# Kernel optimization log

Measured on AMD Instinct MI355X. Metric: run time of the kernel, lower is better.

Reference implementation:

```python
import jax, jax.numpy as jnp
import numpy as np

B = 256          # games in flight
BS = 19          # board side
N2 = BS * BS     # 361 points
M = N2 * 10      # history_factor = 10 -> max moves = 3610


def setup_inputs() -> dict:
    key = jax.random.key(0)
    k = jax.random.split(key, 8)
    legal_mask = jax.random.bernoulli(k[0], 0.5, (B, BS, BS))
    # captures are sparse: few stones captured per candidate move
    capture_stone_mask = jax.random.bernoulli(k[1], 0.02, (B, N2, N2))
    current_player = jax.random.randint(k[2], (B,), 0, 2, dtype=jnp.int32)
    zpos = jax.random.randint(k[3], (N2, 3), 0, 2**31 - 1, dtype=jnp.int32)
    current_hash = jax.random.randint(k[4], (B,), 0, 2**31 - 1, dtype=jnp.int32)
    hash_history = jax.random.randint(k[5], (B, M), 0, 2**31 - 1, dtype=jnp.int32)
    move_count = jax.random.randint(k[6], (B,), 0, M, dtype=jnp.int32)
    logits = jax.random.normal(k[7], (B, BS, BS), dtype=jnp.float32)
    return dict(legal_mask=legal_mask, capture_stone_mask=capture_stone_mask,
                current_player=current_player, zpos=zpos,
                current_hash=current_hash, hash_history=hash_history,
                move_count=move_count, logits=logits)


def _super_ko_filter(legal_mask, capture_stone_mask, current_player, zpos,
                     current_hash, hash_history, move_count):
    Bb, H, W = legal_mask.shape
    n2 = H * W
    legal_flat = legal_mask.reshape(Bb, n2)                      # (B, N2)
    player = current_player.astype(jnp.int32)                    # (B,)
    zposT = zpos.T                                               # (3, N2)

    # 1) delta for placing the stone: empty-key XOR player-key
    place_old = zposT[0][None, :]                                # (1, N2)
    place_new = zposT[player + 1]                                # (B, N2) gather per-batch
    place_delta = jnp.bitwise_xor(place_old, place_new)          # (B, N2)

    # 2) delta for removing a captured opponent stone at each point
    z_opp = zposT[2 - player]                                    # opp+1 = 2-player, (B, N2)
    D = jnp.bitwise_xor(z_opp, zposT[0][None, :])                # (B, N2)

    # per candidate move, XOR the deltas of all stones it would capture
    sel = jnp.where(capture_stone_mask, D[:, None, :], jnp.int32(0))  # (B, N2, N2)
    cap_delta = jax.lax.reduce(sel, jnp.int32(0), jax.lax.bitwise_xor, (2,))  # (B, N2)

    # 3) post-move hash per candidate
    new_hash = current_hash[:, None] ^ place_delta ^ cap_delta   # (B, N2)

    # 4) reject if post-move hash appears in the (valid prefix of) history
    hist_mask = jnp.arange(hash_history.shape[1])[None, :] < move_count[:, None]  # (B, M)
    eq = (new_hash[:, :, None] == hash_history[:, None, :]) & hist_mask[:, None, :]
    is_repeat = jnp.any(eq, axis=2) & legal_flat                 # (B, N2)

    return legal_mask & ~is_repeat.reshape(Bb, H, W)


def reference(legal_mask, capture_stone_mask, current_player, zpos,
              current_hash, hash_history, move_count, logits):
    final_mask = _super_ko_filter(legal_mask, capture_stone_mask, current_player,
                                  zpos, current_hash, hash_history, move_count)
    # downstream use of the filtered mask: mask policy logits
    return jnp.where(final_mask, logits, jnp.float32(-1e9))
```

## Files before the change

kernel.cpp:

```cpp
#include <hip/hip_runtime.h>
#include <stdint.h>


#define GO_B   256
#define GO_N2  361
#define GO_M   3610
#define TBL    1024
#define BTHR   512

__global__ __launch_bounds__(256)
void scan_kernel(const int* __restrict__ cap,
                 const int* __restrict__ player,
                 const int* __restrict__ zpos,
                 uint32_t*  __restrict__ capx_out)
{
    const int b    = blockIdx.x >> 2;
    const int g    = blockIdx.x & 3;
    const int wid  = g * 4 + (threadIdx.x >> 6);
    const int lane = threadIdx.x & 63;
    const int p    = player[b];

    uint32_t D[6];
    #pragma unroll
    for (int s = 0; s < 6; ++s) {
        int j = lane + 64 * s;
        D[s] = (j < GO_N2)
             ? ((uint32_t)zpos[j * 3 + 0] ^ (uint32_t)zpos[j * 3 + 2 - p])
             : 0u;
    }

    const int* __restrict__ base_b = cap + (size_t)b * GO_N2 * GO_N2;

    for (int i = wid; i < GO_N2; i += 32) {
        const int  iB   = i + 16;
        const bool hasB = (iB < GO_N2);
        const int* __restrict__ rowA = base_b + (size_t)i  * GO_N2;
        const int* __restrict__ rowB = base_b + (size_t)iB * GO_N2;

        uint32_t a0, a1, a2, a3, a4, a5;
        uint32_t b0, b1, b2, b3, b4, b5;
        a0 = (uint32_t)rowA[lane];
        a1 = (uint32_t)rowA[lane + 64];
        a2 = (uint32_t)rowA[lane + 128];
        a3 = (uint32_t)rowA[lane + 192];
        a4 = (uint32_t)rowA[lane + 256];
        a5 = (lane + 320 < GO_N2) ? (uint32_t)rowA[lane + 320] : 0u;
        b0 = hasB ? (uint32_t)rowB[lane]       : 0u;
        b1 = hasB ? (uint32_t)rowB[lane + 64]  : 0u;
        b2 = hasB ? (uint32_t)rowB[lane + 128] : 0u;
        b3 = hasB ? (uint32_t)rowB[lane + 192] : 0u;
        b4 = hasB ? (uint32_t)rowB[lane + 256] : 0u;
        b5 = (hasB && lane + 320 < GO_N2) ? (uint32_t)rowB[lane + 320] : 0u;

        uint32_t accA = (a0 ? D[0] : 0u) ^ (a1 ? D[1] : 0u) ^ (a2 ? D[2] : 0u)
                      ^ (a3 ? D[3] : 0u) ^ (a4 ? D[4] : 0u) ^ (a5 ? D[5] : 0u);
        uint32_t accB = (b0 ? D[0] : 0u) ^ (b1 ? D[1] : 0u) ^ (b2 ? D[2] : 0u)
                      ^ (b3 ? D[3] : 0u) ^ (b4 ? D[4] : 0u) ^ (b5 ? D[5] : 0u);

        #pragma unroll
        for (int off = 32; off >= 1; off >>= 1) {
            accA ^= __shfl_xor(accA, off, 64);
            accB ^= __shfl_xor(accB, off, 64);
        }
        if (lane == 0) {
            capx_out[(size_t)b * GO_N2 + i] = accA;
            if (hasB) capx_out[(size_t)b * GO_N2 + iB] = accB;
        }
    }
}

__global__ __launch_bounds__(BTHR)
void finalize_kernel(const int*      __restrict__ legal,
                     const int*      __restrict__ player,
                     const int*      __restrict__ zpos,
                     const int*      __restrict__ chash,
                     const int*      __restrict__ hist,
                     const int*      __restrict__ mcount,
                     const float*    __restrict__ logits,
                     const uint32_t* __restrict__ capx,
                     float*          __restrict__ out)
{
    __shared__ uint32_t thash[TBL];
    __shared__ int      tidx[TBL];
    __shared__ uint8_t  rep[GO_N2];
    __shared__ uint8_t  leg[GO_N2];

    const int b   = blockIdx.x;
    const int tid = threadIdx.x;
    const int p   = player[b];
    const uint32_t ch = (uint32_t)chash[b];

    for (int s = tid; s < TBL; s += BTHR) tidx[s] = -1;
    for (int i = tid; i < GO_N2; i += BTHR) {
        rep[i] = 0u;
        leg[i] = legal[(size_t)b * GO_N2 + i] != 0;
    }
    __syncthreads();

    for (int i = tid; i < GO_N2; i += BTHR) {
        uint32_t z0 = (uint32_t)zpos[i * 3 + 0];
        uint32_t zp = (uint32_t)zpos[i * 3 + 1 + p];
        uint32_t nh = ch ^ (z0 ^ zp) ^ capx[(size_t)b * GO_N2 + i];
        if (leg[i]) {
            uint32_t s = nh & (TBL - 1);
            while (true) {
                int prev = atomicCAS(&tidx[s], -1, i);
                if (prev == -1) { thash[s] = nh; break; }
                s = (s + 1) & (TBL - 1);
            }
        }
    }
    __syncthreads();

    const int mc = mcount[b];
    for (int m = tid; m < mc; m += BTHR) {
        uint32_t h = (uint32_t)hist[(size_t)b * GO_M + m];
        uint32_t s = h & (TBL - 1);
        while (tidx[s] != -1) {
            if (thash[s] == h) rep[tidx[s]] = 1u;
            s = (s + 1) & (TBL - 1);
        }
    }
    __syncthreads();

    for (int i = tid; i < GO_N2; i += BTHR) {
        bool keep = leg[i] && !rep[i];
        out[(size_t)b * GO_N2 + i] =
            keep ? logits[(size_t)b * GO_N2 + i] : -1.0e9f;
    }
}

extern "C" void kernel_launch(void* const* d_in, const int* in_sizes, int n_in,
                              void* d_out, int out_size, void* d_ws, size_t ws_size,
                              hipStream_t stream) {
    const int*   legal  = (const int*)d_in[0];
    const int*   cap    = (const int*)d_in[1];
    const int*   player = (const int*)d_in[2];
    const int*   zpos   = (const int*)d_in[3];
    const int*   chash  = (const int*)d_in[4];
    const int*   hist   = (const int*)d_in[5];
    const int*   mcount = (const int*)d_in[6];
    const float* logits = (const float*)d_in[7];
    float*       outp   = (float*)d_out;
    uint32_t*    capx   = (uint32_t*)d_ws;

    scan_kernel<<<GO_B * 4, 256, 0, stream>>>(cap, player, zpos, capx);
    finalize_kernel<<<GO_B, BTHR, 0, stream>>>(legal, player, zpos, chash,
                                               hist, mcount, logits, capx, outp);
}
```

Before: 237.9 us.

## Stage capture-mask rows through LDS tiles with contiguous loads in scan kernel

```diff
diff --git a/kernel.cpp b/kernel.cpp
--- a/kernel.cpp
+++ b/kernel.cpp
@@ -2,70 +2,80 @@
 #include <stdint.h>
 
 
-#define GO_B   256
-#define GO_N2  361
-#define GO_M   3610
-#define TBL    1024
-#define BTHR   512
+#define GO_B    256
+#define GO_N2   361
+#define GO_M    3610
+#define TBL     1024
+#define BTHR    512
+#define NBLK    8
+#define ROWS_PB 46
+#define TROWS   8
+#define STHR    256
+#define NS      32
+#define CPS     12
 
-__global__ __launch_bounds__(256)
+__global__ __launch_bounds__(STHR)
 void scan_kernel(const int* __restrict__ cap,
                  const int* __restrict__ player,
                  const int* __restrict__ zpos,
-                 uint32_t*  __restrict__ capx_out)
+                 uint32_t*  __restrict__ capx)
 {
-    const int b    = blockIdx.x >> 2;
-    const int g    = blockIdx.x & 3;
-    const int wid  = g * 4 + (threadIdx.x >> 6);
-    const int lane = threadIdx.x & 63;
-    const int p    = player[b];
+    __shared__ uint32_t Dl[GO_N2];
+    __shared__ uint32_t tile[TROWS * GO_N2];
+    __shared__ uint32_t parts[TROWS][NS + 1];
 
-    uint32_t D[6];
-    #pragma unroll
-    for (int s = 0; s < 6; ++s) {
-        int j = lane + 64 * s;
-        D[s] = (j < GO_N2)
-             ? ((uint32_t)zpos[j * 3 + 0] ^ (uint32_t)zpos[j * 3 + 2 - p])
-             : 0u;
-    }
+    const int bq  = blockIdx.x;
+    const int b   = bq >> 3;
+    const int q   = bq & 7;
+    const int tid = threadIdx.x;
+    const int p   = player[b];
 
-    const int* __restrict__ base_b = cap + (size_t)b * GO_N2 * GO_N2;
+    for (int j = tid; j < GO_N2; j += STHR)
+        Dl[j] = (uint32_t)zpos[j * 3 + 0] ^ (uint32_t)zpos[j * 3 + 2 - p];
+    __syncthreads();
 
-    for (int i = wid; i < GO_N2; i += 32) {
-        const int  iB   = i + 16;
-        const bool hasB = (iB < GO_N2);
-        const int* __restrict__ rowA = base_b + (size_t)i  * GO_N2;
-        const int* __restrict__ rowB = base_b + (size_t)iB * GO_N2;
+    const int r0 = q * ROWS_PB;
+    const int r1 = (r0 + ROWS_PB < GO_N2) ? (r0 + ROWS_PB) : GO_N2;
+    const int* __restrict__ slab = cap + (size_t)b * GO_N2 * GO_N2;
 
-        uint32_t a0, a1, a2, a3, a4, a5;
-        uint32_t b0, b1, b2, b3, b4, b5;
-        a0 = (uint32_t)rowA[lane];
-        a1 = (uint32_t)rowA[lane + 64];
-        a2 = (uint32_t)rowA[lane + 128];
-        a3 = (uint32_t)rowA[lane + 192];
-        a4 = (uint32_t)rowA[lane + 256];
-        a5 = (lane + 320 < GO_N2) ? (uint32_t)rowA[lane + 320] : 0u;
-        b0 = hasB ? (uint32_t)rowB[lane]       : 0u;
-        b1 = hasB ? (uint32_t)rowB[lane + 64]  : 0u;
-        b2 = hasB ? (uint32_t)rowB[lane + 128] : 0u;
-        b3 = hasB ? (uint32_t)rowB[lane + 192] : 0u;
-        b4 = hasB ? (uint32_t)rowB[lane + 256] : 0u;
-        b5 = (hasB && lane + 320 < GO_N2) ? (uint32_t)rowB[lane + 320] : 0u;
+    const int r  = tid & (TROWS - 1);
+    const int s  = tid >> 3;
+    const int j0 = s * CPS;
 
-        uint32_t accA = (a0 ? D[0] : 0u) ^ (a1 ? D[1] : 0u) ^ (a2 ? D[2] : 0u)
-                      ^ (a3 ? D[3] : 0u) ^ (a4 ? D[4] : 0u) ^ (a5 ? D[5] : 0u);
-        uint32_t accB = (b0 ? D[0] : 0u) ^ (b1 ? D[1] : 0u) ^ (b2 ? D[2] : 0u)
-                      ^ (b3 ? D[3] : 0u) ^ (b4 ? D[4] : 0u) ^ (b5 ? D[5] : 0u);
+    for (int rt = r0; rt < r1; rt += TROWS) {
+        const int nr  = (TROWS < r1 - rt) ? TROWS : (r1 - rt);
+        const int nel = nr * GO_N2;
+        const int* __restrict__ tsrc = slab + (size_t)rt * GO_N2;
 
-        #pragma unroll
-        for (int off = 32; off >= 1; off >>= 1) {
-            accA ^= __shfl_xor(accA, off, 64);
-            accB ^= __shfl_xor(accB, off, 64);
+        for (int idx = tid; idx < nel; idx += STHR)
+            tile[idx] = (uint32_t)tsrc[idx];
+        __syncthreads();
+
+        uint32_t acc = 0u;
+        if (r < nr) {
+            #pragma unroll
+            for (int c = 0; c < CPS; ++c) {
+                int j = j0 + c;
+                if (j < GO_N2) {
+                    uint32_t m = tile[r * GO_N2 + j];
+                    acc ^= (m ? Dl[j] : 0u);
+                }
+            }
         }
-        if (lane == 0) {
-            capx_out[(size_t)b * GO_N2 + i] = accA;
-            if (hasB) capx_out[(size_t)b * GO_N2 + iB] = accB;
+        parts[r][s] = acc;
+        __syncthreads();
+
+        {
+            const int row = tid >> 5;
+            const int k   = tid & 31;
+            uint32_t v = parts[row][k];
+            #pragma unroll
+            for (int off = 16; off >= 1; off >>= 1)
+                v ^= __shfl_xor(v, off, 32);
+            if (k == 0 && rt + row < r1)
+                capx[(size_t)b * GO_N2 + rt + row] = v;
         }
+        __syncthreads();
     }
 }
 
@@ -144,7 +154,7 @@
     float*       outp   = (float*)d_out;
     uint32_t*    capx   = (uint32_t*)d_ws;
 
-    scan_kernel<<<GO_B * 4, 256, 0, stream>>>(cap, player, zpos, capx);
+    scan_kernel<<<GO_B * NBLK, STHR, 0, stream>>>(cap, player, zpos, capx);
     finalize_kernel<<<GO_B, BTHR, 0, stream>>>(legal, player, zpos, chash,
                                                hist, mcount, logits, capx, outp);
 }
```

Result: faster. 232.7 us (-2.2%).
